# Kernel tuning notes

Hardware: AMD Instinct MI355X
Metric: run time of the kernel (lower is better)

## Reference

```python
import jax, jax.numpy as jnp
import numpy as np

WINDOW = 64
BAND_NUM = 2 * WINDOW      # 128
FILTER_LEN = 6 * WINDOW    # 384


def setup_inputs() -> dict:
    key = jax.random.key(0)
    k1, k2 = jax.random.split(key)
    B, C, T, F = 16, 1, 8192, WINDOW + 1  # F = band_num/2 + 1 = 65
    inp = jax.random.normal(k1, (B, C, T, F), dtype=jnp.float32)
    subband_filter = jax.random.normal(k2, (FILTER_LEN,), dtype=jnp.float32)
    lengths = jnp.full((B,), T, dtype=jnp.int32)  # one sample per batch element, all length T
    return {"input": inp, "subband_filter": subband_filter, "lengths": lengths}


def reference(input, subband_filter, lengths):
    B, C, T, F = input.shape
    S = lengths.shape[0]               # sample_num (static)
    x = input.reshape(-1, F)           # (N, F), N = B*C*T
    # torch.fft.irfft(norm='forward') -> jnp.fft.irfft(norm='forward'), out len = 2*(F-1) = band_num
    ifft_out = jnp.fft.irfft(x, norm='forward')          # (N, 128)
    # tile across the 3 band repeats, apply prototype filter and window gain
    wide = jnp.concatenate([ifft_out, ifft_out, ifft_out], axis=1)  # (N, 384)
    wide = wide * subband_filter[None, :] * WINDOW
    N = wide.shape[0]
    H = N // S                          # in_height (= C*T per sample)
    w = wide.reshape(S, H, 6, WINDOW)   # per-sample, per-frame, 6 taps of width `window`
    true_len = H - 5
    # overlap-add: out[s, t] = sum_k w[s, t + 5 - k, k]
    out = w[:, 5:H, 0, :]
    for k in range(1, 6):
        out = out + w[:, 5 - k:H - k, k, :]
    out = out.reshape(B, C, -1)         # (B, C, true_len*window)
    return out / 32768.0
```

## Files before the change

### kernel.cpp

```cpp
#include <hip/hip_runtime.h>
#include <hip/hip_bf16.h>


#define NF 65
#define NT 8192
#define TRUE_LEN 8187
#define FPW 59
#define WPB 139
#define TABT_STRIDE 36
#define YS_STRIDE 66

typedef const __attribute__((address_space(4))) float cfloat;

__device__ float d_tabT[NF * TABT_STRIDE];

__global__ void build_tab_kernel() {
    int idx = blockIdx.x * 256 + threadIdx.x;
    if (idx >= NF * TABT_STRIDE) return;
    int m = idx / TABT_STRIDE, p = idx % TABT_STRIDE;
    if (p >= 33) { d_tabT[idx] = 0.0f; return; }
    float w = (m == 0 || m == 64) ? 1.0f : 2.0f;
    int a = (m * p) & 127;
    d_tabT[idx] = w * cospif((float)a * (1.0f / 64.0f));
}

__global__ __launch_bounds__(256, 3)
void subband_main_kernel(const float* __restrict__ g_in,
                         const float* __restrict__ g_filt,
                         float* __restrict__ g_out)
{
    __shared__ __hip_bfloat162 Ys2[4][64 * 33];

    const int tid  = threadIdx.x;
    const int lane = tid & 63;
    const int wv   = tid >> 6;
    const int wg   = blockIdx.x * 4 + wv;
    const int s     = wg / WPB;
    const int fbase = (wg % WPB) * FPW;
    int h = fbase + lane;
    if (h > NT - 1) h = NT - 1;

    const float* xr = g_in + ((size_t)s * NT + h) * NF;
    float X[NF];
    #pragma unroll
    for (int c = 0; c < 16; ++c) {
        float t4[4];
        __builtin_memcpy(t4, xr + 4 * c, 16);
        X[4 * c + 0] = t4[0]; X[4 * c + 1] = t4[1];
        X[4 * c + 2] = t4[2]; X[4 * c + 3] = t4[3];
    }
    X[64] = xr[64];

    float E[33], O[33];
    #pragma unroll
    for (int p = 0; p < 33; ++p) { E[p] = 0.0f; O[p] = 0.0f; }

    cfloat* ct = (cfloat*)(unsigned long long)(const float*)d_tabT;
    #pragma unroll
    for (int m = 0; m < NF; ++m) {
        cfloat* c = ct + m * TABT_STRIDE;
        const float xm = X[m];
        float* acc = (m & 1) ? O : E;
        #pragma unroll
        for (int p = 0; p < 33; ++p) acc[p] += c[p] * xm;
    }

    __hip_bfloat162* ys2 = &Ys2[wv][0] + lane * 33;
    #pragma unroll
    for (int q = 0; q < 33; ++q) {
        const int t0 = 2 * q, t1 = 2 * q + 1;
        const float y0 = (t0 <= 32) ? (E[t0] + O[t0]) : (E[64 - t0] - O[64 - t0]);
        const float y1 = (t1 <= 64)
                       ? ((t1 <= 32) ? (E[t1] + O[t1]) : (E[64 - t1] - O[64 - t1]))
                       : 0.0f;
        __hip_bfloat162 pk;
        pk.x = __float2bfloat16(y0);
        pk.y = __float2bfloat16(y1);
        ys2[q] = pk;
    }

    const __hip_bfloat16* ys = (const __hip_bfloat16*)&Ys2[wv][0];
    const int j = lane;
    float fc[6];
    #pragma unroll
    for (int k = 0; k < 6; ++k) fc[k] = g_filt[k * 64 + j] * (1.0f / 512.0f);
    const int te = j;
    const int to = (j == 0) ? 64 : 64 - j;

    float we[6], wo[6];
    #pragma unroll
    for (int r = 0; r < 5; ++r) {
        we[r] = __bfloat162float(ys[r * YS_STRIDE + te]);
        wo[r] = __bfloat162float(ys[r * YS_STRIDE + to]);
    }
    float* dst = g_out + ((size_t)s * TRUE_LEN + fbase) * 64 + j;

    #pragma unroll
    for (int q = 0; q < FPW; ++q) {
        if (fbase + q >= TRUE_LEN) break;
        we[5] = __bfloat162float(ys[(q + 5) * YS_STRIDE + te]);
        wo[5] = __bfloat162float(ys[(q + 5) * YS_STRIDE + to]);
        const float o = fc[0] * we[5] + fc[1] * wo[4] + fc[2] * we[3]
                      + fc[3] * wo[2] + fc[4] * we[1] + fc[5] * wo[0];
        dst[(size_t)q * 64] = o;
        #pragma unroll
        for (int r = 0; r < 5; ++r) { we[r] = we[r + 1]; wo[r] = wo[r + 1]; }
    }
}

extern "C" void kernel_launch(void* const* d_in, const int* in_sizes, int n_in,
                              void* d_out, int out_size, void* d_ws, size_t ws_size,
                              hipStream_t stream) {
    const float* g_in   = (const float*)d_in[0];
    const float* g_filt = (const float*)d_in[1];
    float* g_out = (float*)d_out;

    build_tab_kernel<<<10, 256, 0, stream>>>();
    subband_main_kernel<<<556, 256, 0, stream>>>(g_in, g_filt, g_out);
}
```

Before: 108.4 us.

## Split even/odd DCT across two waves per chunk with shared-memory staging

Restructures the main kernel so each 128-thread block handles one 59-frame chunk with two wavefronts. The input tile is loaded cooperatively into shared memory, one wave computes the even-index partial sums and the other the odd ones, and both then combine and overlap-add halves of the frames. This reduces per-thread register pressure (33 accumulators instead of 66, 33 inputs instead of 65) and coalesces the global input loads. In exchange it adds several block barriers and extra shared-memory traffic, and it doubles the number of wavefronts that repeat the table reads.

```diff
diff --git a/kernel.cpp b/kernel.cpp
--- a/kernel.cpp
+++ b/kernel.cpp
@@ -6,103 +6,132 @@
 #define NT 8192
 #define TRUE_LEN 8187
 #define FPW 59
-#define WPB 139
-#define TABT_STRIDE 36
-#define YS_STRIDE 66
+#define CPB 139
+#define XSTR 67
+#define TSTR 36
+#define EOSTR 34
+#define YSTR 66
 
 typedef const __attribute__((address_space(4))) float cfloat;
 
-__device__ float d_tabT[NF * TABT_STRIDE];
+__device__ float d_tab[2 * 33 * TSTR];
 
 __global__ void build_tab_kernel() {
     int idx = blockIdx.x * 256 + threadIdx.x;
-    if (idx >= NF * TABT_STRIDE) return;
-    int m = idx / TABT_STRIDE, p = idx % TABT_STRIDE;
-    if (p >= 33) { d_tabT[idx] = 0.0f; return; }
-    float w = (m == 0 || m == 64) ? 1.0f : 2.0f;
-    int a = (m * p) & 127;
-    d_tabT[idx] = w * cospif((float)a * (1.0f / 64.0f));
+    if (idx >= 2 * 33 * TSTR) return;
+    int par = idx / (33 * TSTR);
+    int rem = idx - par * 33 * TSTR;
+    int p = rem / TSTR, n = rem - p * TSTR;
+    int m = 2 * n + par;
+    float v = 0.0f;
+    if (n < 33 && m <= 64) {
+        float w = (m == 0 || m == 64) ? 1.0f : 2.0f;
+        int a = (m * p) & 127;
+        v = w * cospif((float)a * (1.0f / 64.0f));
+    }
+    d_tab[idx] = v;
 }
 
-__global__ __launch_bounds__(256, 3)
+__global__ __launch_bounds__(128, 4)
 void subband_main_kernel(const float* __restrict__ g_in,
                          const float* __restrict__ g_filt,
                          float* __restrict__ g_out)
 {
-    __shared__ __hip_bfloat162 Ys2[4][64 * 33];
+    __shared__ float smem[64 * XSTR];
+    __hip_bfloat16* Es = (__hip_bfloat16*)smem;
+    __hip_bfloat16* Os = (__hip_bfloat16*)((char*)smem + 4352);
+    __hip_bfloat16* Yb = (__hip_bfloat16*)((char*)smem + 8704);
 
     const int tid  = threadIdx.x;
     const int lane = tid & 63;
     const int wv   = tid >> 6;
-    const int wg   = blockIdx.x * 4 + wv;
-    const int s     = wg / WPB;
-    const int fbase = (wg % WPB) * FPW;
-    int h = fbase + lane;
-    if (h > NT - 1) h = NT - 1;
+    const int cg   = blockIdx.x;
+    const int s     = cg / CPB;
+    const int fbase = (cg - s * CPB) * FPW;
 
-    const float* xr = g_in + ((size_t)s * NT + h) * NF;
-    float X[NF];
+    const float* src = g_in + (size_t)s * NT * NF;
+    for (int i = tid; i < 64 * NF; i += 128) {
+        int r = i / NF, c = i - r * NF;
+        int h = fbase + r; if (h > NT - 1) h = NT - 1;
+        smem[r * XSTR + c] = src[(size_t)h * NF + c];
+    }
+    { int r = tid >> 1, sl = NF + (tid & 1); smem[r * XSTR + sl] = 0.0f; }
+    __syncthreads();
+
+    const int row = lane;
+    float Xr[33];
     #pragma unroll
-    for (int c = 0; c < 16; ++c) {
-        float t4[4];
-        __builtin_memcpy(t4, xr + 4 * c, 16);
-        X[4 * c + 0] = t4[0]; X[4 * c + 1] = t4[1];
-        X[4 * c + 2] = t4[2]; X[4 * c + 3] = t4[3];
+    for (int n = 0; n < 33; ++n) Xr[n] = smem[row * XSTR + 2 * n + wv];
+    __syncthreads();
+
+    const int tab_off = __builtin_amdgcn_readfirstlane(wv * (33 * TSTR));
+    cfloat* ct = (cfloat*)(unsigned long long)(const float*)(d_tab + tab_off);
+    __hip_bfloat16* eo = (wv == 0) ? Es : Os;
+    for (int p = 0; p < 33; ++p) {
+        cfloat* cf = ct + p * TSTR;
+        float a0 = 0.0f, a1 = 0.0f, a2 = 0.0f, a3 = 0.0f;
+        #pragma unroll
+        for (int n = 0; n < 32; n += 4) {
+            a0 += cf[n]     * Xr[n];
+            a1 += cf[n + 1] * Xr[n + 1];
+            a2 += cf[n + 2] * Xr[n + 2];
+            a3 += cf[n + 3] * Xr[n + 3];
+        }
+        a0 += cf[32] * Xr[32];
+        eo[row * EOSTR + p] = __float2bfloat16((a0 + a2) + (a1 + a3));
     }
-    X[64] = xr[64];
+    __syncthreads();
 
-    float E[33], O[33];
-    #pragma unroll
-    for (int p = 0; p < 33; ++p) { E[p] = 0.0f; O[p] = 0.0f; }
+    {
+        const int crow = wv * 32 + (lane & 31);
+        const int g = lane >> 5;
+        for (int it = 0; it < 17; ++it) {
+            const int q = g * 17 + it;
+            if (q > 32) break;
+            const int t0 = 2 * q, t1 = 2 * q + 1;
+            const int p0 = (t0 <= 32) ? t0 : 64 - t0;
+            const float e0 = __bfloat162float(Es[crow * EOSTR + p0]);
+            const float o0 = __bfloat162float(Os[crow * EOSTR + p0]);
+            const float y0 = (t0 <= 32) ? e0 + o0 : e0 - o0;
+            float y1 = 0.0f;
+            if (t1 <= 64) {
+                const int p1 = (t1 <= 32) ? t1 : 64 - t1;
+                const float e1 = __bfloat162float(Es[crow * EOSTR + p1]);
+                const float o1 = __bfloat162float(Os[crow * EOSTR + p1]);
+                y1 = (t1 <= 32) ? e1 + o1 : e1 - o1;
+            }
+            __hip_bfloat162 pk;
+            pk.x = __float2bfloat16(y0);
+            pk.y = __float2bfloat16(y1);
+            *(__hip_bfloat162*)&Yb[crow * YSTR + t0] = pk;
+        }
+    }
+    __syncthreads();
 
-    cfloat* ct = (cfloat*)(unsigned long long)(const float*)d_tabT;
-    #pragma unroll
-    for (int m = 0; m < NF; ++m) {
-        cfloat* c = ct + m * TABT_STRIDE;
-        const float xm = X[m];
-        float* acc = (m & 1) ? O : E;
-        #pragma unroll
-        for (int p = 0; p < 33; ++p) acc[p] += c[p] * xm;
-    }
-
-    __hip_bfloat162* ys2 = &Ys2[wv][0] + lane * 33;
-    #pragma unroll
-    for (int q = 0; q < 33; ++q) {
-        const int t0 = 2 * q, t1 = 2 * q + 1;
-        const float y0 = (t0 <= 32) ? (E[t0] + O[t0]) : (E[64 - t0] - O[64 - t0]);
-        const float y1 = (t1 <= 64)
-                       ? ((t1 <= 32) ? (E[t1] + O[t1]) : (E[64 - t1] - O[64 - t1]))
-                       : 0.0f;
-        __hip_bfloat162 pk;
-        pk.x = __float2bfloat16(y0);
-        pk.y = __float2bfloat16(y1);
-        ys2[q] = pk;
-    }
-
-    const __hip_bfloat16* ys = (const __hip_bfloat16*)&Ys2[wv][0];
     const int j = lane;
     float fc[6];
     #pragma unroll
     for (int k = 0; k < 6; ++k) fc[k] = g_filt[k * 64 + j] * (1.0f / 512.0f);
     const int te = j;
     const int to = (j == 0) ? 64 : 64 - j;
+    const int qlo = wv * 30;
+    const int nq  = 30 - wv;
 
     float we[6], wo[6];
     #pragma unroll
     for (int r = 0; r < 5; ++r) {
-        we[r] = __bfloat162float(ys[r * YS_STRIDE + te]);
-        wo[r] = __bfloat162float(ys[r * YS_STRIDE + to]);
+        we[r] = __bfloat162float(Yb[(qlo + r) * YSTR + te]);
+        wo[r] = __bfloat162float(Yb[(qlo + r) * YSTR + to]);
     }
-    float* dst = g_out + ((size_t)s * TRUE_LEN + fbase) * 64 + j;
+    float* dst = g_out + ((size_t)s * TRUE_LEN + fbase + qlo) * 64 + j;
 
-    #pragma unroll
-    for (int q = 0; q < FPW; ++q) {
-        if (fbase + q >= TRUE_LEN) break;
-        we[5] = __bfloat162float(ys[(q + 5) * YS_STRIDE + te]);
-        wo[5] = __bfloat162float(ys[(q + 5) * YS_STRIDE + to]);
+    for (int u = 0; u < nq; ++u) {
+        if (fbase + qlo + u >= TRUE_LEN) break;
+        we[5] = __bfloat162float(Yb[(qlo + u + 5) * YSTR + te]);
+        wo[5] = __bfloat162float(Yb[(qlo + u + 5) * YSTR + to]);
         const float o = fc[0] * we[5] + fc[1] * wo[4] + fc[2] * we[3]
                       + fc[3] * wo[2] + fc[4] * we[1] + fc[5] * wo[0];
-        dst[(size_t)q * 64] = o;
+        dst[(size_t)u * 64] = o;
         #pragma unroll
         for (int r = 0; r < 5; ++r) { we[r] = we[r + 1]; wo[r] = wo[r + 1]; }
     }
@@ -116,5 +145,5 @@
     float* g_out = (float*)d_out;
 
     build_tab_kernel<<<10, 256, 0, stream>>>();
-    subband_main_kernel<<<556, 256, 0, stream>>>(g_in, g_filt, g_out);
+    subband_main_kernel<<<16 * CPB, 128, 0, stream>>>(g_in, g_filt, g_out);
 }
```

After: 105.8 us. -2.4%, faster.
